# Kernel tuning notes

Measured on AMD Instinct MI355X. Metric: run time of the kernel, lower is better.

## Reference

```python
import jax, jax.numpy as jnp
import numpy as np

N_NODES = 50000
N_EDGES = 1600000
N_FEAT = 512
N_HID = 256
N_CLS = 64
K_HOPS = 10
ALPHA = 0.1


def setup_inputs() -> dict:
    key = jax.random.key(0)
    k1, k2, k3, k4 = jax.random.split(key, 4)
    x = jax.random.normal(k1, (N_NODES, N_FEAT), dtype=jnp.float32)
    edge_index = jax.random.randint(k2, (2, N_EDGES), 0, N_NODES, dtype=jnp.int64)
    W1 = jax.random.normal(k3, (N_HID, N_FEAT), dtype=jnp.float32) * (1.0 / np.sqrt(N_FEAT))
    W2 = jax.random.normal(k4, (N_CLS, N_HID), dtype=jnp.float32) * (1.0 / np.sqrt(N_HID))
    return {"x": x, "edge_index": edge_index, "W1": W1, "W2": W2}


def reference(x, edge_index, W1, W2):
    n = x.shape[0]
    # --- MLP encoder (eval mode: dropout is identity) ---
    hidden = jax.nn.relu(x @ W1.T)            # [N, n_hidden]
    out = hidden @ W2.T                        # [N, n_classes]

    # --- GCN normalization with self-loops (PyG gcn_norm defaults) ---
    loops = jnp.arange(n, dtype=edge_index.dtype)
    src = jnp.concatenate([edge_index[0], loops])  # [E+N]
    dst = jnp.concatenate([edge_index[1], loops])  # [E+N]
    deg = jax.ops.segment_sum(jnp.ones_like(src, dtype=out.dtype), dst, num_segments=n)
    dinv = jnp.where(deg > 0, jax.lax.rsqrt(deg), 0.0)
    norm = dinv[src] * dinv[dst]                   # [E+N]

    # --- APPNP: K hops of propagate + teleport blend ---
    h0 = out
    for _ in range(K_HOPS):
        msg = norm[:, None] * out[src]                         # gather [E+N, C]
        agg = jax.ops.segment_sum(msg, dst, num_segments=n)    # scatter-add [N, C]
        out = (1.0 - ALPHA) * agg + ALPHA * h0

    return jax.nn.log_softmax(out, axis=1)
```

## Files before the change

kernel.cpp:

```cpp
#include <hip/hip_runtime.h>
#include <hip/hip_bf16.h>
#include <cstdint>
#include <cstddef>

#define N_NODES 50000
#define N_EDGES 1600000
#define N_FEAT  512
#define N_HID   256
#define N_CLS   64
#define K_HOPS  10
#define NPAD    50016
#define DUMMY   N_NODES
#define P16(d) (((d) + 15) & ~15)
#define STAGE_CAP 256
#define HOP_GRID 3125
#define G1_BLOCKS 782
#define DEG_BLOCKS 1563
#define G2_BLOCKS 391
#define SCAT_BLOCKS 1563

typedef __attribute__((ext_vector_type(4))) float f32x4;
typedef __attribute__((ext_vector_type(4))) int   i32x4;
typedef __attribute__((ext_vector_type(2))) unsigned int u32x2;
typedef __attribute__((ext_vector_type(4))) unsigned short u16x4;
typedef __attribute__((ext_vector_type(8))) short s16x8;

__device__ __forceinline__ ushort f2bf(float f) {
    uint32_t u = __float_as_uint(f);
    uint32_t r = (u + 0x7FFFu + ((u >> 16) & 1u)) >> 16;
    return (ushort)r;
}

__device__ __forceinline__ uint32_t cvtpk(float a, float b) {
    uint32_t r;
    asm("v_cvt_pk_bf16_f32 %0, %1, %2" : "=v"(r) : "v"(a), "v"(b));
    return r;
}

__device__ __forceinline__ f32x4 bf4_to_f32(u16x4 v) {
    f32x4 r;
    r[0] = __uint_as_float((uint32_t)v[0] << 16);
    r[1] = __uint_as_float((uint32_t)v[1] << 16);
    r[2] = __uint_as_float((uint32_t)v[2] << 16);
    r[3] = __uint_as_float((uint32_t)v[3] << 16);
    return r;
}

__launch_bounds__(256)
__global__ void g1deg_k(const float* __restrict__ X, const float* __restrict__ W1,
                        ushort* __restrict__ H, const int* __restrict__ dst,
                        int* __restrict__ deg, int* __restrict__ pos) {
    __shared__ ushort sA[128 * 64];
    __shared__ ushort sB[128 * 64];
    const int bid = blockIdx.x;
    const int t = threadIdx.x;

    if (bid >= G1_BLOCKS) {
        int e = ((bid - G1_BLOCKS) * 256 + t) * 4;
        if (e + 3 < N_EDGES) {
            const i32x4 d = __builtin_nontemporal_load(
                reinterpret_cast<const i32x4*>(dst + e));
            i32x4 p;
            p[0] = atomicAdd(&deg[d[0]], 1);
            p[1] = atomicAdd(&deg[d[1]], 1);
            p[2] = atomicAdd(&deg[d[2]], 1);
            p[3] = atomicAdd(&deg[d[3]], 1);
            __builtin_nontemporal_store(p, reinterpret_cast<i32x4*>(pos + e));
        } else {
            for (int k = 0; k < 4 && e + k < N_EDGES; ++k)
                pos[e + k] = atomicAdd(&deg[dst[e + k]], 1);
        }
        return;
    }

    const int m0 = (bid >> 1) * 128;
    const int n0 = (bid & 1) * 128;
    const int wid = t >> 6, lane = t & 63;
    const int wr = wid >> 1, wc = wid & 1;
    const int lo = lane & 15, hi = lane >> 4;

    f32x4 acc[4][4] = {};

    for (int kt = 0; kt < N_FEAT; kt += 64) {
        #pragma unroll
        for (int p = 0; p < 8; ++p) {
            int idx = p * 256 + t;
            int row = idx >> 4, f4 = idx & 15;
            int grow = m0 + row; if (grow > N_NODES - 1) grow = N_NODES - 1;
            const float4 v = *reinterpret_cast<const float4*>(X + (size_t)grow * N_FEAT + kt + f4 * 4);
            uint2 h; h.x = cvtpk(v.x, v.y); h.y = cvtpk(v.z, v.w);
            int g = f4 >> 1;
            int off = row * 64 + ((g ^ (row & 7)) << 3) + ((f4 & 1) << 2);
            *reinterpret_cast<uint2*>(&sA[off]) = h;
        }
        #pragma unroll
        for (int p = 0; p < 8; ++p) {
            int idx = p * 256 + t;
            int row = idx >> 4, f4 = idx & 15;
            const float4 v = *reinterpret_cast<const float4*>(W1 + (size_t)(n0 + row) * N_FEAT + kt + f4 * 4);
            uint2 h; h.x = cvtpk(v.x, v.y); h.y = cvtpk(v.z, v.w);
            int g = f4 >> 1;
            int off = row * 64 + ((g ^ (row & 7)) << 3) + ((f4 & 1) << 2);
            *reinterpret_cast<uint2*>(&sB[off]) = h;
        }
        __syncthreads();
        #pragma unroll
        for (int kk = 0; kk < 2; ++kk) {
            const int g = kk * 4 + hi;
            s16x8 a[4], b[4];
            #pragma unroll
            for (int i = 0; i < 4; ++i) {
                int row = wr * 64 + i * 16 + lo;
                a[i] = *reinterpret_cast<const s16x8*>(&sA[row * 64 + ((g ^ (row & 7)) << 3)]);
            }
            #pragma unroll
            for (int j = 0; j < 4; ++j) {
                int row = wc * 64 + j * 16 + lo;
                b[j] = *reinterpret_cast<const s16x8*>(&sB[row * 64 + ((g ^ (row & 7)) << 3)]);
            }
            #pragma unroll
            for (int i = 0; i < 4; ++i)
                #pragma unroll
                for (int j = 0; j < 4; ++j)
                    acc[i][j] = __builtin_amdgcn_mfma_f32_16x16x32_bf16(a[i], b[j], acc[i][j], 0, 0, 0);
        }
        __syncthreads();
    }
    #pragma unroll
    for (int i = 0; i < 4; ++i) {
        int rbase = m0 + wr * 64 + i * 16 + hi * 4;
        #pragma unroll
        for (int j = 0; j < 4; ++j) {
            int col = n0 + wc * 64 + j * 16 + lo;
            #pragma unroll
            for (int r = 0; r < 4; ++r) {
                int row = rbase + r;
                if (row < N_NODES) {
                    float v = acc[i][j][r];
                    H[(size_t)row * N_HID + col] = f2bf(fmaxf(v, 0.0f));
                }
            }
        }
    }
}

__device__ __forceinline__ int wave_incl_scan(int v, int lane) {
    #pragma unroll
    for (int d = 1; d < 64; d <<= 1) {
        int u = __shfl_up(v, d, 64);
        if (lane >= d) v += u;
    }
    return v;
}

__global__ void dsc1_k(const int* __restrict__ deg, float* __restrict__ dinv,
                       float* __restrict__ rd, int* __restrict__ partial) {
    int i = blockIdx.x * 256 + threadIdx.x;
    int d = (i < N_NODES) ? deg[i] : 0;
    if (i < N_NODES) {
        float dp1 = (float)d + 1.0f;
        dinv[i] = rsqrtf(dp1);
        rd[i]   = sqrtf(dp1);
    }
    int v = (i < N_NODES) ? P16(d) : 0;
    #pragma unroll
    for (int s = 32; s; s >>= 1) v += __shfl_xor(v, s, 64);
    __shared__ int wt[4];
    int wid = threadIdx.x >> 6, lane = threadIdx.x & 63;
    if (lane == 0) wt[wid] = v;
    __syncthreads();
    if (threadIdx.x == 0) partial[blockIdx.x] = wt[0] + wt[1] + wt[2] + wt[3];
}

__global__ void sc2_k(const int* __restrict__ partial, int* __restrict__ chunkoff,
                      int* __restrict__ row_ptr, ushort* __restrict__ b0,
                      ushort* __restrict__ b1, ushort* __restrict__ b2) {
    int t = threadIdx.x;
    int v = (t < 196) ? partial[t] : 0;
    int lane = t & 63, wid = t >> 6;
    int incl = wave_incl_scan(v, lane);
    __shared__ int wt[4];
    if (lane == 63) wt[wid] = incl;
    __syncthreads();
    int woff = 0;
    for (int w = 0; w < wid; ++w) woff += wt[w];
    int excl = incl - v + woff;
    if (t < 196) chunkoff[t] = excl;
    if (t == 0) row_ptr[N_NODES] = wt[0] + wt[1] + wt[2] + wt[3];
    if (t < 192) {
        ushort* b = (t < 64) ? b0 : (t < 128) ? b1 : b2;
        b[(size_t)DUMMY * 64 + (t & 63)] = 0;
    }
}

__global__ void sc3_k(const int* __restrict__ cnt, const int* __restrict__ chunkoff,
                      int* __restrict__ row_ptr, int* __restrict__ csr) {
    int i = blockIdx.x * 256 + threadIdx.x;
    int dg = (i < N_NODES) ? cnt[i] : 0;
    int v = (i < N_NODES) ? P16(dg) : 0;
    int lane = threadIdx.x & 63, wid = threadIdx.x >> 6;
    int incl = wave_incl_scan(v, lane);
    __shared__ int wt[4];
    if (lane == 63) wt[wid] = incl;
    __syncthreads();
    int woff = 0;
    for (int w = 0; w < wid; ++w) woff += wt[w];
    int excl = incl - v + woff;
    if (i < N_NODES) {
        int rp = chunkoff[blockIdx.x] + excl;
        row_ptr[i] = rp;
        int base = rp + dg;
        int pad = P16(dg) - dg;
        for (int k = 0; k < pad; ++k) csr[base + k] = DUMMY;
    }
}

__launch_bounds__(256)
__global__ void scg2_k(const ushort* __restrict__ H, const float* __restrict__ W2,
                       const float* __restrict__ dinv, ushort* __restrict__ out,
                       const int* __restrict__ src, const int* __restrict__ dst,
                       const int* __restrict__ pos, const int* __restrict__ row_ptr,
                       int* __restrict__ csr) {
    __shared__ ushort sA[128 * 64];
    __shared__ ushort sB[64 * 64];
    const int bid = blockIdx.x;
    const int t = threadIdx.x;

    if (bid >= G2_BLOCKS) {
        int e = ((bid - G2_BLOCKS) * 256 + t) * 4;
        if (e + 3 < N_EDGES) {
            const i32x4 d4 = __builtin_nontemporal_load(
                reinterpret_cast<const i32x4*>(dst + e));
            const i32x4 s4 = __builtin_nontemporal_load(
                reinterpret_cast<const i32x4*>(src + e));
            const i32x4 p4 = __builtin_nontemporal_load(
                reinterpret_cast<const i32x4*>(pos + e));
            #pragma unroll
            for (int k = 0; k < 4; ++k)
                csr[row_ptr[d4[k]] + p4[k]] = s4[k];
        } else {
            for (int k = 0; k < 4 && e + k < N_EDGES; ++k)
                csr[row_ptr[dst[e + k]] + pos[e + k]] = src[e + k];
        }
        return;
    }

    const int m0 = bid * 128;
    const int wid = t >> 6, lane = t & 63;
    const int lo = lane & 15, hi = lane >> 4;

    f32x4 acc[2][4] = {};

    for (int kt = 0; kt < N_HID; kt += 64) {
        #pragma unroll
        for (int p = 0; p < 4; ++p) {
            int idx = p * 256 + t;
            int row = idx >> 3, g = idx & 7;
            int grow = m0 + row; if (grow > N_NODES - 1) grow = N_NODES - 1;
            uint4 v = *reinterpret_cast<const uint4*>(H + (size_t)grow * N_HID + kt + g * 8);
            *reinterpret_cast<uint4*>(&sA[row * 64 + ((g ^ (row & 7)) << 3)]) = v;
        }
        #pragma unroll
        for (int p = 0; p < 4; ++p) {
            int idx = p * 256 + t;
            int row = idx >> 4, f4 = idx & 15;
            const float4 v = *reinterpret_cast<const float4*>(W2 + (size_t)row * N_HID + kt + f4 * 4);
            uint2 h; h.x = cvtpk(v.x, v.y); h.y = cvtpk(v.z, v.w);
            int g = f4 >> 1;
            int off = row * 64 + ((g ^ (row & 7)) << 3) + ((f4 & 1) << 2);
            *reinterpret_cast<uint2*>(&sB[off]) = h;
        }
        __syncthreads();
        #pragma unroll
        for (int kk = 0; kk < 2; ++kk) {
            const int g = kk * 4 + hi;
            s16x8 a[2], b[4];
            #pragma unroll
            for (int i = 0; i < 2; ++i) {
                int row = wid * 32 + i * 16 + lo;
                a[i] = *reinterpret_cast<const s16x8*>(&sA[row * 64 + ((g ^ (row & 7)) << 3)]);
            }
            #pragma unroll
            for (int j = 0; j < 4; ++j) {
                int row = j * 16 + lo;
                b[j] = *reinterpret_cast<const s16x8*>(&sB[row * 64 + ((g ^ (row & 7)) << 3)]);
            }
            #pragma unroll
            for (int i = 0; i < 2; ++i)
                #pragma unroll
                for (int j = 0; j < 4; ++j)
                    acc[i][j] = __builtin_amdgcn_mfma_f32_16x16x32_bf16(a[i], b[j], acc[i][j], 0, 0, 0);
        }
        __syncthreads();
    }
    #pragma unroll
    for (int i = 0; i < 2; ++i) {
        int rbase = m0 + wid * 32 + i * 16 + hi * 4;
        #pragma unroll
        for (int r = 0; r < 4; ++r) {
            int row = rbase + r;
            if (row < N_NODES) {
                const float dv = dinv[row];
                #pragma unroll
                for (int j = 0; j < 4; ++j)
                    out[(size_t)row * 64 + j * 16 + lo] = f2bf(acc[i][j][r] * dv);
            }
        }
    }
}

__launch_bounds__(256)
__global__ void hop_k(const ushort* __restrict__ prev, const ushort* __restrict__ h0,
                      ushort* __restrict__ next, const int* __restrict__ csr,
                      const int* __restrict__ row_ptr, const float* __restrict__ dinv) {
    __shared__ int scsr[4][STAGE_CAP];
    const int bid = blockIdx.x;
    const int wid = threadIdx.x >> 6;
    const int lane = threadIdx.x & 63;
    const int nb = bid * 16 + wid * 4;
    const int slot = lane >> 4;
    const int cq = (lane & 15) << 2;

    const int b0 = __builtin_amdgcn_readfirstlane(row_ptr[nb]);
    const int e0 = __builtin_amdgcn_readfirstlane(row_ptr[nb + 1]);
    const int e1 = __builtin_amdgcn_readfirstlane(row_ptr[nb + 2]);
    const int e2 = __builtin_amdgcn_readfirstlane(row_ptr[nb + 3]);
    const int e3 = __builtin_amdgcn_readfirstlane(row_ptr[nb + 4]);
    const int tot = e3 - b0;

    int* sw = scsr[wid];
    #pragma unroll
    for (int k = 0; k < 4; ++k) {
        int off = k * 64 + lane;
        if (off < tot && off < STAGE_CAP)
            sw[off] = __builtin_nontemporal_load(csr + b0 + off);
    }

    f32x4 a0 = {0.f,0.f,0.f,0.f}, a1 = a0, a2 = a0, a3 = a0;

#define NODE_LOOP(Bg, Eg, ACC)                                                   \
    {                                                                            \
        int ib = (Bg);                                                           \
        for (; ib + 32 <= (Eg); ib += 32) {                                      \
            int s[8];                                                            \
            if (ib + 32 - b0 <= STAGE_CAP) {                                     \
                int base = ib - b0 + slot;                                       \
                _Pragma("unroll")                                                \
                for (int k = 0; k < 8; ++k) s[k] = sw[base + 4 * k];             \
            } else {                                                             \
                _Pragma("unroll")                                                \
                for (int k = 0; k < 8; ++k)                                      \
                    s[k] = __builtin_nontemporal_load(csr + ib + slot + 4 * k);  \
            }                                                                    \
            u16x4 p[8];                                                          \
            _Pragma("unroll")                                                    \
            for (int k = 0; k < 8; ++k)                                          \
                p[k] = *reinterpret_cast<const u16x4*>(prev + (size_t)s[k] * 64 + cq); \
            _Pragma("unroll")                                                    \
            for (int k = 0; k < 8; ++k) {                                        \
                const f32x4 f = bf4_to_f32(p[k]);                                \
                ACC[0] += f[0]; ACC[1] += f[1]; ACC[2] += f[2]; ACC[3] += f[3];  \
            }                                                                    \
        }                                                                        \
        if (ib < (Eg)) {                                                         \
            int s[4];                                                            \
            if (ib + 16 - b0 <= STAGE_CAP) {                                     \
                int base = ib - b0 + slot;                                       \
                _Pragma("unroll")                                                \
                for (int k = 0; k < 4; ++k) s[k] = sw[base + 4 * k];             \
            } else {                                                             \
                _Pragma("unroll")                                                \
                for (int k = 0; k < 4; ++k)                                      \
                    s[k] = __builtin_nontemporal_load(csr + ib + slot + 4 * k);  \
            }                                                                    \
            u16x4 p[4];                                                          \
            _Pragma("unroll")                                                    \
            for (int k = 0; k < 4; ++k)                                          \
                p[k] = *reinterpret_cast<const u16x4*>(prev + (size_t)s[k] * 64 + cq); \
            _Pragma("unroll")                                                    \
            for (int k = 0; k < 4; ++k) {                                        \
                const f32x4 f = bf4_to_f32(p[k]);                                \
                ACC[0] += f[0]; ACC[1] += f[1]; ACC[2] += f[2]; ACC[3] += f[3];  \
            }                                                                    \
        }                                                                        \
    }

    NODE_LOOP(b0, e0, a0)
    NODE_LOOP(e0, e1, a1)
    NODE_LOOP(e1, e2, a2)
    NODE_LOOP(e2, e3, a3)
#undef NODE_LOOP

    #pragma unroll
    for (int c = 0; c < 4; ++c) {
        a0[c] += __shfl_xor(a0[c], 16, 64); a0[c] += __shfl_xor(a0[c], 32, 64);
        a1[c] += __shfl_xor(a1[c], 16, 64); a1[c] += __shfl_xor(a1[c], 32, 64);
        a2[c] += __shfl_xor(a2[c], 16, 64); a2[c] += __shfl_xor(a2[c], 32, 64);
        a3[c] += __shfl_xor(a3[c], 16, 64); a3[c] += __shfl_xor(a3[c], 32, 64);
    }

    {
        const int node = nb + slot;
        const float di = dinv[node];
        const float di2 = di * di;
        f32x4 av = a0;
        if (slot == 1) av = a1;
        if (slot == 2) av = a2;
        if (slot == 3) av = a3;
        const size_t off = (size_t)node * 64 + cq;
        const f32x4 pv = bf4_to_f32(*reinterpret_cast<const u16x4*>(prev + off));
        const f32x4 hh = bf4_to_f32(__builtin_nontemporal_load(
            reinterpret_cast<const u16x4*>(h0 + off)));
        float r0 = 0.9f * di2 * (av[0] + pv[0]) + 0.1f * hh[0];
        float r1 = 0.9f * di2 * (av[1] + pv[1]) + 0.1f * hh[1];
        float r2 = 0.9f * di2 * (av[2] + pv[2]) + 0.1f * hh[2];
        float r3 = 0.9f * di2 * (av[3] + pv[3]) + 0.1f * hh[3];
        u32x2 o;
        o[0] = cvtpk(r0, r1);
        o[1] = cvtpk(r2, r3);
        __builtin_nontemporal_store(o, reinterpret_cast<u32x2*>(next + off));
    }
}

__launch_bounds__(256)
__global__ void logsm_k(const ushort* __restrict__ in, const float* __restrict__ rd,
                        float* __restrict__ out) {
    int r = (blockIdx.x * 256 + threadIdx.x) >> 6;
    int lane = threadIdx.x & 63;
    if (r >= N_NODES) return;
    float v = __uint_as_float((uint32_t)in[(size_t)r * 64 + lane] << 16) * rd[r];
    float m = v;
    #pragma unroll
    for (int d = 32; d; d >>= 1) m = fmaxf(m, __shfl_xor(m, d, 64));
    float e = __expf(v - m);
    float s = e;
    #pragma unroll
    for (int d = 32; d; d >>= 1) s += __shfl_xor(s, d, 64);
    out[(size_t)r * N_CLS + lane] = (v - m) - __logf(s);
}

extern "C" void kernel_launch(void* const* d_in, const int* in_sizes, int n_in,
                              void* d_out, int out_size, void* d_ws, size_t ws_size,
                              hipStream_t stream) {
    const float* X  = (const float*)d_in[0];
    const int*   EI = (const int*)d_in[1];
    const float* W1 = (const float*)d_in[2];
    const float* W2 = (const float*)d_in[3];
    const int* src = EI;
    const int* dst = EI + N_EDGES;

    char* ws = (char*)d_ws;
    ushort* H      = (ushort*)(ws + 0);
    int*    csr    = (int*)  (ws + 25600000);
    int*    deg    = (int*)  (ws + 35200000);
    float*  dinv   = (float*)(ws + 35400000);
    float*  rd     = (float*)(ws + 35600000);
    int*    rptr   = (int*)  (ws + 35800000);
    int*    part   = (int*)  (ws + 36000016);
    int*    coff   = (int*)  (ws + 36001024);
    int*    pos    = (int*)  (ws + 36002048);
    ushort* h0t    = (ushort*)(ws + 42402048);
    ushort* pp0    = (ushort*)(ws + 48804096);
    ushort* pp1    = (ushort*)(ws + 55206144);

    hipMemsetAsync(deg, 0, N_NODES * sizeof(int), stream);

    g1deg_k<<<G1_BLOCKS + DEG_BLOCKS, 256, 0, stream>>>(X, W1, H, dst, deg, pos);

    dsc1_k<<<196, 256, 0, stream>>>(deg, dinv, rd, part);
    sc2_k<<<1, 256, 0, stream>>>(part, coff, rptr, h0t, pp0, pp1);
    sc3_k<<<196, 256, 0, stream>>>(deg, coff, rptr, csr);

    scg2_k<<<G2_BLOCKS + SCAT_BLOCKS, 256, 0, stream>>>(H, W2, dinv, h0t,
                                                        src, dst, pos, rptr, csr);

    const ushort* p = h0t;
    ushort* bufs[2] = {pp0, pp1};
    for (int k = 0; k < K_HOPS; ++k) {
        ushort* nx = bufs[k & 1];
        hop_k<<<HOP_GRID, 256, 0, stream>>>(p, h0t, nx, csr, rptr, dinv);
        p = nx;
    }
    logsm_k<<<12500, 256, 0, stream>>>(p, rd, (float*)d_out);
}
```

Baseline: 406.7 us.

## Use 16-bit CSR indices, fold self-loop into CSR, widen hop gathers

Stores CSR column indices as ushort instead of int, which halves index traffic in the scatter and in all ten hop kernels. The self-loop is placed inside the CSR row, so the hop no longer re-reads the previous value separately. Hop lanes now gather 8 bf16 values (16 bytes) per neighbour with 8 slots instead of 4, at the cost of an extra shuffle-reduction stage. The degree blocks are also moved ahead of the GEMM blocks in the fused launch. The ushort indices only work because node ids stay below 65536, and the padding rule changes so every row holds at least one extra slot.

```diff
diff --git a/kernel.cpp b/kernel.cpp
--- a/kernel.cpp
+++ b/kernel.cpp
@@ -11,18 +11,19 @@
 #define K_HOPS  10
 #define NPAD    50016
 #define DUMMY   N_NODES
-#define P16(d) (((d) + 15) & ~15)
+#define PS(d)   (((d) + 16) & ~15)
 #define STAGE_CAP 256
 #define HOP_GRID 3125
+#define DEG_BLOCKS 1563
 #define G1_BLOCKS 782
-#define DEG_BLOCKS 1563
 #define G2_BLOCKS 391
 #define SCAT_BLOCKS 1563
 
 typedef __attribute__((ext_vector_type(4))) float f32x4;
 typedef __attribute__((ext_vector_type(4))) int   i32x4;
-typedef __attribute__((ext_vector_type(2))) unsigned int u32x2;
+typedef __attribute__((ext_vector_type(4))) unsigned int   u32x4;
 typedef __attribute__((ext_vector_type(4))) unsigned short u16x4;
+typedef __attribute__((ext_vector_type(8))) unsigned short u16x8;
 typedef __attribute__((ext_vector_type(8))) short s16x8;
 
 __device__ __forceinline__ ushort f2bf(float f) {
@@ -37,13 +38,8 @@
     return r;
 }
 
-__device__ __forceinline__ f32x4 bf4_to_f32(u16x4 v) {
-    f32x4 r;
-    r[0] = __uint_as_float((uint32_t)v[0] << 16);
-    r[1] = __uint_as_float((uint32_t)v[1] << 16);
-    r[2] = __uint_as_float((uint32_t)v[2] << 16);
-    r[3] = __uint_as_float((uint32_t)v[3] << 16);
-    return r;
+__device__ __forceinline__ float bfe(ushort v) {
+    return __uint_as_float((uint32_t)v << 16);
 }
 
 __launch_bounds__(256)
@@ -55,8 +51,8 @@
     const int bid = blockIdx.x;
     const int t = threadIdx.x;
 
-    if (bid >= G1_BLOCKS) {
-        int e = ((bid - G1_BLOCKS) * 256 + t) * 4;
+    if (bid < DEG_BLOCKS) {
+        int e = (bid * 256 + t) * 4;
         if (e + 3 < N_EDGES) {
             const i32x4 d = __builtin_nontemporal_load(
                 reinterpret_cast<const i32x4*>(dst + e));
@@ -73,8 +69,9 @@
         return;
     }
 
-    const int m0 = (bid >> 1) * 128;
-    const int n0 = (bid & 1) * 128;
+    const int b2 = bid - DEG_BLOCKS;
+    const int m0 = (b2 >> 1) * 128;
+    const int n0 = (b2 & 1) * 128;
     const int wid = t >> 6, lane = t & 63;
     const int wr = wid >> 1, wc = wid & 1;
     const int lo = lane & 15, hi = lane >> 4;
@@ -162,7 +159,7 @@
         dinv[i] = rsqrtf(dp1);
         rd[i]   = sqrtf(dp1);
     }
-    int v = (i < N_NODES) ? P16(d) : 0;
+    int v = (i < N_NODES) ? PS(d) : 0;
     #pragma unroll
     for (int s = 32; s; s >>= 1) v += __shfl_xor(v, s, 64);
     __shared__ int wt[4];
@@ -194,10 +191,10 @@
 }
 
 __global__ void sc3_k(const int* __restrict__ cnt, const int* __restrict__ chunkoff,
-                      int* __restrict__ row_ptr, int* __restrict__ csr) {
+                      int* __restrict__ row_ptr, ushort* __restrict__ csr) {
     int i = blockIdx.x * 256 + threadIdx.x;
     int dg = (i < N_NODES) ? cnt[i] : 0;
-    int v = (i < N_NODES) ? P16(dg) : 0;
+    int v = (i < N_NODES) ? PS(dg) : 0;
     int lane = threadIdx.x & 63, wid = threadIdx.x >> 6;
     int incl = wave_incl_scan(v, lane);
     __shared__ int wt[4];
@@ -210,8 +207,9 @@
         int rp = chunkoff[blockIdx.x] + excl;
         row_ptr[i] = rp;
         int base = rp + dg;
-        int pad = P16(dg) - dg;
-        for (int k = 0; k < pad; ++k) csr[base + k] = DUMMY;
+        csr[base] = (ushort)i;
+        int pad = PS(dg) - dg;
+        for (int k = 1; k < pad; ++k) csr[base + k] = (ushort)DUMMY;
     }
 }
 
@@ -220,7 +218,7 @@
                        const float* __restrict__ dinv, ushort* __restrict__ out,
                        const int* __restrict__ src, const int* __restrict__ dst,
                        const int* __restrict__ pos, const int* __restrict__ row_ptr,
-                       int* __restrict__ csr) {
+                       ushort* __restrict__ csr) {
     __shared__ ushort sA[128 * 64];
     __shared__ ushort sB[64 * 64];
     const int bid = blockIdx.x;
@@ -237,10 +235,10 @@
                 reinterpret_cast<const i32x4*>(pos + e));
             #pragma unroll
             for (int k = 0; k < 4; ++k)
-                csr[row_ptr[d4[k]] + p4[k]] = s4[k];
+                csr[row_ptr[d4[k]] + p4[k]] = (ushort)s4[k];
         } else {
             for (int k = 0; k < 4 && e + k < N_EDGES; ++k)
-                csr[row_ptr[dst[e + k]] + pos[e + k]] = src[e + k];
+                csr[row_ptr[dst[e + k]] + pos[e + k]] = (ushort)src[e + k];
         }
         return;
     }
@@ -311,15 +309,15 @@
 
 __launch_bounds__(256)
 __global__ void hop_k(const ushort* __restrict__ prev, const ushort* __restrict__ h0,
-                      ushort* __restrict__ next, const int* __restrict__ csr,
+                      ushort* __restrict__ next, const ushort* __restrict__ csr,
                       const int* __restrict__ row_ptr, const float* __restrict__ dinv) {
-    __shared__ int scsr[4][STAGE_CAP];
+    __shared__ ushort scsr[4][STAGE_CAP];
     const int bid = blockIdx.x;
     const int wid = threadIdx.x >> 6;
     const int lane = threadIdx.x & 63;
     const int nb = bid * 16 + wid * 4;
-    const int slot = lane >> 4;
-    const int cq = (lane & 15) << 2;
+    const int slot = lane >> 3;
+    const int cl8 = (lane & 7) << 3;
 
     const int b0 = __builtin_amdgcn_readfirstlane(row_ptr[nb]);
     const int e0 = __builtin_amdgcn_readfirstlane(row_ptr[nb + 1]);
@@ -328,97 +326,105 @@
     const int e3 = __builtin_amdgcn_readfirstlane(row_ptr[nb + 4]);
     const int tot = e3 - b0;
 
-    int* sw = scsr[wid];
-    #pragma unroll
-    for (int k = 0; k < 4; ++k) {
-        int off = k * 64 + lane;
-        if (off < tot && off < STAGE_CAP)
-            sw[off] = __builtin_nontemporal_load(csr + b0 + off);
-    }
-
-    f32x4 a0 = {0.f,0.f,0.f,0.f}, a1 = a0, a2 = a0, a3 = a0;
-
-#define NODE_LOOP(Bg, Eg, ACC)                                                   \
+    ushort* sw = scsr[wid];
+    {
+        int off4 = lane * 4;
+        if (off4 < tot && off4 < STAGE_CAP) {
+            u16x4 v = __builtin_nontemporal_load(
+                reinterpret_cast<const u16x4*>(csr + b0 + off4));
+            *reinterpret_cast<u16x4*>(&sw[off4]) = v;
+        }
+    }
+
+    f32x4 a00 = {0.f,0.f,0.f,0.f}, a01 = a00;
+    f32x4 a10 = a00, a11 = a00, a20 = a00, a21 = a00, a30 = a00, a31 = a00;
+
+#define ADD8(A0, A1, P)                                                          \
+    { A0[0] += bfe(P[0]); A0[1] += bfe(P[1]); A0[2] += bfe(P[2]); A0[3] += bfe(P[3]); \
+      A1[0] += bfe(P[4]); A1[1] += bfe(P[5]); A1[2] += bfe(P[6]); A1[3] += bfe(P[7]); }
+
+#define NODE_LOOP(Bg, Eg, A0, A1)                                                \
     {                                                                            \
         int ib = (Bg);                                                           \
         for (; ib + 32 <= (Eg); ib += 32) {                                      \
-            int s[8];                                                            \
+            int s[4];                                                            \
             if (ib + 32 - b0 <= STAGE_CAP) {                                     \
                 int base = ib - b0 + slot;                                       \
                 _Pragma("unroll")                                                \
-                for (int k = 0; k < 8; ++k) s[k] = sw[base + 4 * k];             \
+                for (int k = 0; k < 4; ++k) s[k] = sw[base + 8 * k];             \
             } else {                                                             \
                 _Pragma("unroll")                                                \
-                for (int k = 0; k < 8; ++k)                                      \
-                    s[k] = __builtin_nontemporal_load(csr + ib + slot + 4 * k);  \
+                for (int k = 0; k < 4; ++k)                                      \
+                    s[k] = __builtin_nontemporal_load(csr + ib + slot + 8 * k);  \
             }                                                                    \
-            u16x4 p[8];                                                          \
+            u16x8 p[4];                                                          \
             _Pragma("unroll")                                                    \
-            for (int k = 0; k < 8; ++k)                                          \
-                p[k] = *reinterpret_cast<const u16x4*>(prev + (size_t)s[k] * 64 + cq); \
+            for (int k = 0; k < 4; ++k)                                          \
+                p[k] = *reinterpret_cast<const u16x8*>(prev + (size_t)s[k] * 64 + cl8); \
             _Pragma("unroll")                                                    \
-            for (int k = 0; k < 8; ++k) {                                        \
-                const f32x4 f = bf4_to_f32(p[k]);                                \
-                ACC[0] += f[0]; ACC[1] += f[1]; ACC[2] += f[2]; ACC[3] += f[3];  \
-            }                                                                    \
+            for (int k = 0; k < 4; ++k) ADD8(A0, A1, p[k])                       \
         }                                                                        \
         if (ib < (Eg)) {                                                         \
-            int s[4];                                                            \
+            int s[2];                                                            \
             if (ib + 16 - b0 <= STAGE_CAP) {                                     \
                 int base = ib - b0 + slot;                                       \
                 _Pragma("unroll")                                                \
-                for (int k = 0; k < 4; ++k) s[k] = sw[base + 4 * k];             \
+                for (int k = 0; k < 2; ++k) s[k] = sw[base + 8 * k];             \
             } else {                                                             \
                 _Pragma("unroll")                                                \
-                for (int k = 0; k < 4; ++k)                                      \
-                    s[k] = __builtin_nontemporal_load(csr + ib + slot + 4 * k);  \
+                for (int k = 0; k < 2; ++k)                                      \
+                    s[k] = __builtin_nontemporal_load(csr + ib + slot + 8 * k);  \
             }                                                                    \
-            u16x4 p[4];                                                          \
+            u16x8 p[2];                                                          \
             _Pragma("unroll")                                                    \
-            for (int k = 0; k < 4; ++k)                                          \
-                p[k] = *reinterpret_cast<const u16x4*>(prev + (size_t)s[k] * 64 + cq); \
+            for (int k = 0; k < 2; ++k)                                          \
+                p[k] = *reinterpret_cast<const u16x8*>(prev + (size_t)s[k] * 64 + cl8); \
             _Pragma("unroll")                                                    \
-            for (int k = 0; k < 4; ++k) {                                        \
-                const f32x4 f = bf4_to_f32(p[k]);                                \
-                ACC[0] += f[0]; ACC[1] += f[1]; ACC[2] += f[2]; ACC[3] += f[3];  \
-            }                                                                    \
+            for (int k = 0; k < 2; ++k) ADD8(A0, A1, p[k])                       \
         }                                                                        \
     }
 
-    NODE_LOOP(b0, e0, a0)
-    NODE_LOOP(e0, e1, a1)
-    NODE_LOOP(e1, e2, a2)
-    NODE_LOOP(e2, e3, a3)
+    NODE_LOOP(b0, e0, a00, a01)
+    NODE_LOOP(e0, e1, a10, a11)
+    NODE_LOOP(e1, e2, a20, a21)
+    NODE_LOOP(e2, e3, a30, a31)
 #undef NODE_LOOP
 
     #pragma unroll
     for (int c = 0; c < 4; ++c) {
-        a0[c] += __shfl_xor(a0[c], 16, 64); a0[c] += __shfl_xor(a0[c], 32, 64);
-        a1[c] += __shfl_xor(a1[c], 16, 64); a1[c] += __shfl_xor(a1[c], 32, 64);
-        a2[c] += __shfl_xor(a2[c], 16, 64); a2[c] += __shfl_xor(a2[c], 32, 64);
-        a3[c] += __shfl_xor(a3[c], 16, 64); a3[c] += __shfl_xor(a3[c], 32, 64);
-    }
-
-    {
+        a00[c] += __shfl_xor(a00[c], 8, 64); a00[c] += __shfl_xor(a00[c], 16, 64); a00[c] += __shfl_xor(a00[c], 32, 64);
+        a01[c] += __shfl_xor(a01[c], 8, 64); a01[c] += __shfl_xor(a01[c], 16, 64); a01[c] += __shfl_xor(a01[c], 32, 64);
+        a10[c] += __shfl_xor(a10[c], 8, 64); a10[c] += __shfl_xor(a10[c], 16, 64); a10[c] += __shfl_xor(a10[c], 32, 64);
+        a11[c] += __shfl_xor(a11[c], 8, 64); a11[c] += __shfl_xor(a11[c], 16, 64); a11[c] += __shfl_xor(a11[c], 32, 64);
+        a20[c] += __shfl_xor(a20[c], 8, 64); a20[c] += __shfl_xor(a20[c], 16, 64); a20[c] += __shfl_xor(a20[c], 32, 64);
+        a21[c] += __shfl_xor(a21[c], 8, 64); a21[c] += __shfl_xor(a21[c], 16, 64); a21[c] += __shfl_xor(a21[c], 32, 64);
+        a30[c] += __shfl_xor(a30[c], 8, 64); a30[c] += __shfl_xor(a30[c], 16, 64); a30[c] += __shfl_xor(a30[c], 32, 64);
+        a31[c] += __shfl_xor(a31[c], 8, 64); a31[c] += __shfl_xor(a31[c], 16, 64); a31[c] += __shfl_xor(a31[c], 32, 64);
+    }
+
+    if (slot < 4) {
         const int node = nb + slot;
         const float di = dinv[node];
-        const float di2 = di * di;
-        f32x4 av = a0;
-        if (slot == 1) av = a1;
-        if (slot == 2) av = a2;
-        if (slot == 3) av = a3;
-        const size_t off = (size_t)node * 64 + cq;
-        const f32x4 pv = bf4_to_f32(*reinterpret_cast<const u16x4*>(prev + off));
-        const f32x4 hh = bf4_to_f32(__builtin_nontemporal_load(
-            reinterpret_cast<const u16x4*>(h0 + off)));
-        float r0 = 0.9f * di2 * (av[0] + pv[0]) + 0.1f * hh[0];
-        float r1 = 0.9f * di2 * (av[1] + pv[1]) + 0.1f * hh[1];
-        float r2 = 0.9f * di2 * (av[2] + pv[2]) + 0.1f * hh[2];
-        float r3 = 0.9f * di2 * (av[3] + pv[3]) + 0.1f * hh[3];
-        u32x2 o;
-        o[0] = cvtpk(r0, r1);
-        o[1] = cvtpk(r2, r3);
-        __builtin_nontemporal_store(o, reinterpret_cast<u32x2*>(next + off));
+        const float w = 0.9f * di * di;
+        f32x4 av0 = a00, av1 = a01;
+        if (slot == 1) { av0 = a10; av1 = a11; }
+        if (slot == 2) { av0 = a20; av1 = a21; }
+        if (slot == 3) { av0 = a30; av1 = a31; }
+        const size_t off = (size_t)node * 64 + cl8;
+        const u16x8 hh = __builtin_nontemporal_load(
+            reinterpret_cast<const u16x8*>(h0 + off));
+        float r0 = w * av0[0] + 0.1f * bfe(hh[0]);
+        float r1 = w * av0[1] + 0.1f * bfe(hh[1]);
+        float r2 = w * av0[2] + 0.1f * bfe(hh[2]);
+        float r3 = w * av0[3] + 0.1f * bfe(hh[3]);
+        float r4 = w * av1[0] + 0.1f * bfe(hh[4]);
+        float r5 = w * av1[1] + 0.1f * bfe(hh[5]);
+        float r6 = w * av1[2] + 0.1f * bfe(hh[6]);
+        float r7 = w * av1[3] + 0.1f * bfe(hh[7]);
+        u32x4 o;
+        o[0] = cvtpk(r0, r1); o[1] = cvtpk(r2, r3);
+        o[2] = cvtpk(r4, r5); o[3] = cvtpk(r6, r7);
+        __builtin_nontemporal_store(o, reinterpret_cast<u32x4*>(next + off));
     }
 }
 
@@ -451,21 +457,21 @@
 
     char* ws = (char*)d_ws;
     ushort* H      = (ushort*)(ws + 0);
-    int*    csr    = (int*)  (ws + 25600000);
-    int*    deg    = (int*)  (ws + 35200000);
-    float*  dinv   = (float*)(ws + 35400000);
-    float*  rd     = (float*)(ws + 35600000);
-    int*    rptr   = (int*)  (ws + 35800000);
-    int*    part   = (int*)  (ws + 36000016);
-    int*    coff   = (int*)  (ws + 36001024);
-    int*    pos    = (int*)  (ws + 36002048);
-    ushort* h0t    = (ushort*)(ws + 42402048);
-    ushort* pp0    = (ushort*)(ws + 48804096);
-    ushort* pp1    = (ushort*)(ws + 55206144);
+    ushort* csr    = (ushort*)(ws + 25600000);
+    int*    deg    = (int*)  (ws + 30600000);
+    float*  dinv   = (float*)(ws + 30800000);
+    float*  rd     = (float*)(ws + 31000000);
+    int*    rptr   = (int*)  (ws + 31200000);
+    int*    part   = (int*)  (ws + 31400016);
+    int*    coff   = (int*)  (ws + 31401024);
+    int*    pos    = (int*)  (ws + 31402048);
+    ushort* h0t    = (ushort*)(ws + 37802048);
+    ushort* pp0    = (ushort*)(ws + 44204096);
+    ushort* pp1    = (ushort*)(ws + 50606144);
 
     hipMemsetAsync(deg, 0, N_NODES * sizeof(int), stream);
 
-    g1deg_k<<<G1_BLOCKS + DEG_BLOCKS, 256, 0, stream>>>(X, W1, H, dst, deg, pos);
+    g1deg_k<<<DEG_BLOCKS + G1_BLOCKS, 256, 0, stream>>>(X, W1, H, dst, deg, pos);
 
     dsc1_k<<<196, 256, 0, stream>>>(deg, dinv, rd, part);
     sc2_k<<<1, 256, 0, stream>>>(part, coff, rptr, h0t, pp0, pp1);
```

Result: slower. 490.1 us (+20.5%).
